# Kernel optimization log

Hardware: AMD Instinct MI355X
Metric: run time of the kernel (lower is better)

Reference implementation:

```python
import jax, jax.numpy as jnp
import numpy as np

B, N, L, K = 32, 512, 8, 8


def setup_inputs() -> dict:
    key = jax.random.key(0)
    k1, k2 = jax.random.split(key)
    A = jax.random.normal(k1, (B, N, N), dtype=jnp.float32)
    A = 0.5 * (A + A.transpose(0, 2, 1))  # symmetric matrix, as in MMF use-case
    O_stack = jax.random.normal(k2, (L, B, K, K), dtype=jnp.float32)  # per-level KxK rotations
    rng = np.random.default_rng(0)
    idx = np.stack([np.sort(rng.choice(N, K, replace=False)) for _ in range(B * L)])
    indices = jnp.asarray(idx.reshape(B, L, K), dtype=jnp.int32)  # sorted, distinct per (b,l)
    wavelet = indices[:, :, 0]  # wavelet index is one of the selected indices per level
    return {"A": A, "O_stack": O_stack, "indices": indices, "wavelet": wavelet}


def reference(A, O_stack, indices, wavelet):
    Bz, Nz, _ = A.shape
    Lz = O_stack.shape[0]
    eye = jnp.eye(Nz, dtype=A.dtype)

    def build_U(idx, O):
        # identity except the KxK block at (idx_i, idx_j) replaced by O
        # (matches torch boolean-mask row-major fill since idx is sorted)
        return eye.at[idx[:, None], idx[None, :]].set(O)

    right = None
    for l in range(Lz):
        U = jax.vmap(build_U)(indices[:, l], O_stack[l])  # [B,N,N]
        right = U if l == 0 else U @ right
        A = U @ A @ U.transpose(0, 2, 1)

    # final masking: zero rows/cols of wavelet indices, keep diagonal
    active = jnp.ones((Bz, Nz), dtype=A.dtype).at[jnp.arange(Bz)[:, None], wavelet].set(0.0)
    left = active[:, :, None] * active[:, None, :]
    d = jnp.arange(Nz)
    left = left.at[:, d, d].set(1.0)
    D = A * left
    A_rec = right.transpose(0, 2, 1) @ D @ right
    return (A_rec, right, D)
```

## Files before the change

### kernel.cpp

```cpp
#include <hip/hip_runtime.h>

#define BATCH 32
#define NDIM 512
#define LNUM 8
#define KDIM 8

#define WS_PM     0
#define WS_S      512
#define WS_ACT    640
#define WS_W      1152
#define WS_B2     5248
#define WS_C2     9344
#define WS_RA     13440
#define WS_RD     46208
#define WS_RAT    78976
#define WS_RDT    111744
#define WS_STRIDE 144512

#define LSTR 65
typedef float f4 __attribute__((ext_vector_type(4)));

__global__ __launch_bounds__(256) void k_prep(
    const float* __restrict__ A, const float* __restrict__ O,
    const int* __restrict__ indices, const int* __restrict__ wavelet,
    float* __restrict__ ws)
{
    const int b  = blockIdx.x;
    const int cy = blockIdx.y;
    const int tid = threadIdx.x;
    float* base = ws + (size_t)b * WS_STRIDE;

    __shared__ float Wl[64*LSTR];
    __shared__ __align__(16) float Buf1[64*LSTR];
    __shared__ __align__(16) float Buf2[64*LSTR];
    __shared__ __align__(16) float Buf3[64*LSTR];
    __shared__ int   pml[NDIM];
    __shared__ float actl[NDIM];
    __shared__ float actS[64];
    __shared__ int   idxsh[64];
    __shared__ int   Ssh[64];
    __shared__ float Oall[LNUM*KDIM*KDIM];

    for (int t = tid; t < LNUM*KDIM*KDIM; t += 256) {
        int l = t >> 6, k = t & 63;
        Oall[t] = O[((size_t)l*BATCH + b)*(KDIM*KDIM) + k];
    }
    if (tid < 64) idxsh[tid] = indices[b*64 + tid];
    for (int n = tid; n < NDIM; n += 256) { pml[n] = -1; actl[n] = 1.f; }
    __syncthreads();

    const int wv = tid >> 6;
    const int ln = tid & 63;
    int s_reg = 0;

    if (wv == 0) {
        int n = idxsh[ln];
        bool first = true;
        for (int t = 0; t < ln; ++t) if (idxsh[t] == n) first = false;
        unsigned long long m = __ballot(first);
        int rank = __popcll(m & ((1ull << ln) - 1ull));
        s_reg = (int)__popcll(m);
        if (first) { pml[n] = rank; Ssh[rank] = n; }
        if (ln >= s_reg) Ssh[ln] = 0;
        if (ln < LNUM) actl[wavelet[b*LNUM + ln]] = 0.f;
    }
    __syncthreads();

    if (wv == 0) {
        actS[ln] = actl[Ssh[ln]];
        for (int rr = 0; rr < 64; ++rr)
            Wl[rr*LSTR + ln] = (rr == ln && rr < s_reg) ? 1.f : 0.f;
        for (int l = 0; l < LNUM; ++l) {
            int pr[KDIM];
            float wcol[KDIM], accv[KDIM];
            #pragma unroll
            for (int j = 0; j < KDIM; ++j) pr[j] = pml[idxsh[l*KDIM + j]];
            #pragma unroll
            for (int j = 0; j < KDIM; ++j) wcol[j] = Wl[pr[j]*LSTR + ln];
            #pragma unroll
            for (int i = 0; i < KDIM; ++i) {
                float a = 0.f;
                #pragma unroll
                for (int j = 0; j < KDIM; ++j)
                    a += Oall[l*64 + i*KDIM + j] * wcol[j];
                accv[i] = a;
            }
            #pragma unroll
            for (int i = 0; i < KDIM; ++i) Wl[pr[i]*LSTR + ln] = accv[i];
        }
    } else {
        if (cy < 8) {
            const int j0 = cy * 64;
            for (int t = tid - 64; t < 1024; t += 192) {
                int n = t >> 4, cc = t & 15;
                f4 v = ((const f4*)(A + ((size_t)b*NDIM + Ssh[n])*NDIM + j0))[cc];
                ((f4*)(Buf1 + n*64))[cc] = v;
            }
        } else {
            for (int t = tid - 64; t < 4096; t += 192) {
                int n = t >> 6, mm = t & 63;
                Buf1[n*LSTR + mm] = A[((size_t)b*NDIM + Ssh[n])*NDIM + Ssh[mm]];
            }
            int*   g_posmap = (int*)(base + WS_PM);
            float* g_act    = base + WS_ACT;
            for (int n = tid - 64; n < NDIM; n += 192) {
                g_posmap[n] = pml[n]; g_act[n] = actl[n];
            }
        }
    }
    __syncthreads();

    if (cy < 8) {
        const int j0 = cy * 64;
        float* AS  = Buf1;
        float* RAt = Buf2;
        float* g_RA  = base + WS_RA;
        float* g_RD  = base + WS_RD;
        float* g_RAT = base + WS_RAT;
        float* g_RDT = base + WS_RDT;

        const int g = wv;
        const int j = ln;
        float racc[16];

        #pragma unroll
        for (int k = 0; k < 16; ++k) racc[k] = 0.f;
        for (int n = 0; n < 64; ++n) {
            float av = AS[n*64 + j];
            #pragma unroll
            for (int k = 0; k < 16; ++k) racc[k] += Wl[(g*16 + k)*LSTR + n] * av;
        }
        #pragma unroll
        for (int k = 0; k < 16; ++k) {
            RAt[(g*16 + k)*64 + j] = racc[k];
            g_RA[(g*16 + k)*NDIM + j0 + j] = racc[k];
        }
        {
            f4* dst = (f4*)(g_RAT + (size_t)(j0 + j)*64 + g*16);
            #pragma unroll
            for (int q = 0; q < 4; ++q) {
                f4 v = { racc[4*q], racc[4*q+1], racc[4*q+2], racc[4*q+3] };
                dst[q] = v;
            }
        }
        __syncthreads();

        #pragma unroll
        for (int k = 0; k < 16; ++k) racc[k] = 0.f;
        for (int n = 0; n < 64; ++n) {
            float dt = actS[n] * RAt[n*64 + j];
            #pragma unroll
            for (int k = 0; k < 16; ++k) racc[k] += Wl[n*LSTR + g*16 + k] * dt;
        }
        const float aj = actl[j0 + j];
        #pragma unroll
        for (int k = 0; k < 16; ++k) {
            float rd = racc[k] * aj;
            racc[k] = rd;
            g_RD[(g*16 + k)*NDIM + j0 + j] = rd;
        }
        {
            f4* dst = (f4*)(g_RDT + (size_t)(j0 + j)*64 + g*16);
            #pragma unroll
            for (int q = 0; q < 4; ++q) {
                f4 v = { racc[4*q], racc[4*q+1], racc[4*q+2], racc[4*q+3] };
                dst[q] = v;
            }
        }
    } else {
        {
            float* g_W = base + WS_W;
            for (int t = tid; t < 4096; t += 256) g_W[t] = Wl[(t>>6)*LSTR + (t&63)];
        }

        const int w = wv;
        float acc[16];

        #pragma unroll
        for (int k = 0; k < 16; ++k) acc[k] = 0.f;
        for (int n = 0; n < 64; ++n) {
            float as = Buf1[n*LSTR + ln];
            #pragma unroll
            for (int k = 0; k < 16; ++k) acc[k] += Wl[(w*16 + k)*LSTR + n] * as;
        }
        #pragma unroll
        for (int k = 0; k < 16; ++k) Buf2[(w*16 + k)*LSTR + ln] = acc[k];
        __syncthreads();

        #pragma unroll
        for (int k = 0; k < 16; ++k) acc[k] = 0.f;
        for (int m = 0; m < 64; ++m) {
            float wvv = Wl[ln*LSTR + m];
            #pragma unroll
            for (int k = 0; k < 16; ++k) acc[k] += Buf2[(w*16 + k)*LSTR + m] * wvv;
        }
        #pragma unroll
        for (int k = 0; k < 16; ++k) Buf3[(w*16 + k)*LSTR + ln] = acc[k];
        __syncthreads();
        {
            float* g_B2 = base + WS_B2;
            for (int t = tid; t < 4096; t += 256) g_B2[t] = Buf3[(t>>6)*LSTR + (t&63)];
        }

        for (int t = tid; t < 4096; t += 256) {
            int n = t >> 6, m = t & 63;
            float mv = (Ssh[n] == Ssh[m]) ? 1.f : actS[n]*actS[m];
            Buf1[n*LSTR + m] = mv * Buf3[n*LSTR + m];
        }
        __syncthreads();

        #pragma unroll
        for (int k = 0; k < 16; ++k) acc[k] = 0.f;
        for (int n = 0; n < 64; ++n) {
            float dv = Buf1[n*LSTR + ln];
            #pragma unroll
            for (int k = 0; k < 16; ++k) acc[k] += Wl[n*LSTR + (w*16 + k)] * dv;
        }
        #pragma unroll
        for (int k = 0; k < 16; ++k) Buf2[(w*16 + k)*LSTR + ln] = acc[k];
        __syncthreads();

        #pragma unroll
        for (int k = 0; k < 16; ++k) acc[k] = 0.f;
        for (int m = 0; m < 64; ++m) {
            float wvv = Wl[m*LSTR + ln];
            #pragma unroll
            for (int k = 0; k < 16; ++k) acc[k] += Buf2[(w*16 + k)*LSTR + m] * wvv;
        }
        {
            float* g_C2 = base + WS_C2;
            #pragma unroll
            for (int k = 0; k < 16; ++k) g_C2[(w*16 + k)*64 + ln] = acc[k];
        }
    }
}

__global__ __launch_bounds__(256) void k_big(const float* __restrict__ A,
                                             const float* __restrict__ ws,
                                             float* __restrict__ out)
{
    const int b = blockIdx.y;
    const int rh = threadIdx.x >> 7;
    const int lane = threadIdx.x & 127;
    const int i = blockIdx.x*2 + rh;
    const int j0 = lane*4;

    const float* base = ws + (size_t)b * WS_STRIDE;
    const int*   posmap = (const int*)(base + WS_PM);
    const float* act = base + WS_ACT;
    const float* g_W  = base + WS_W;
    const float* g_B2 = base + WS_B2;
    const float* g_C2 = base + WS_C2;
    const float* RA  = base + WS_RA;
    const float* RD  = base + WS_RD;
    const float* RAT = base + WS_RAT;
    const float* RDT = base + WS_RDT;

    const int pi = posmap[i];
    const float acti = act[i];
    const size_t rowoff = ((size_t)b*NDIM + i)*NDIM;
    const size_t seg = (size_t)BATCH*NDIM*NDIM;

    int4   p4  = ((const int4*)posmap)[lane];
    float4 aj4 = ((const float4*)act)[lane];
    int   pm[4] = {p4.x, p4.y, p4.z, p4.w};
    float aj[4] = {aj4.x, aj4.y, aj4.z, aj4.w};

    float a[4], arec[4], dv[4], rv[4];

    if (pi < 0) {
        const float* rat = RAT + (size_t)i*64;
        const float* rdt = RDT + (size_t)i*64;
        f4 v = __builtin_nontemporal_load((const f4*)(A + rowoff) + lane);
        a[0]=v.x; a[1]=v.y; a[2]=v.z; a[3]=v.w;
        #pragma unroll
        for (int c = 0; c < 4; ++c) {
            int pj = pm[c];
            if (pj >= 0) a[c] = rat[pj];
            float mv = (i == j0 + c) ? 1.f : acti * aj[c];
            dv[c] = a[c] * mv;
            arec[c] = (pj < 0) ? dv[c] : rdt[pj];
            rv[c] = (i == j0 + c) ? 1.f : 0.f;
        }
    } else {
        f4 v = ((const f4*)(RA + (size_t)pi*NDIM))[lane];
        f4 w = ((const f4*)(RD + (size_t)pi*NDIM))[lane];
        a[0]=v.x; a[1]=v.y; a[2]=v.z; a[3]=v.w;
        arec[0]=w.x; arec[1]=w.y; arec[2]=w.z; arec[3]=w.w;
        #pragma unroll
        for (int c = 0; c < 4; ++c) {
            int pj = pm[c];
            if (pj >= 0) {
                a[c]    = g_B2[pi*64 + pj];
                arec[c] = g_C2[pi*64 + pj];
                rv[c]   = g_W[pi*64 + pj];
            } else {
                rv[c] = 0.f;
            }
            float mv = (i == j0 + c) ? 1.f : acti * aj[c];
            dv[c] = a[c] * mv;
        }
    }

    f4 o0; o0.x = arec[0]; o0.y = arec[1]; o0.z = arec[2]; o0.w = arec[3];
    f4 o1; o1.x = rv[0];   o1.y = rv[1];   o1.z = rv[2];   o1.w = rv[3];
    f4 o2; o2.x = dv[0];   o2.y = dv[1];   o2.z = dv[2];   o2.w = dv[3];
    __builtin_nontemporal_store(o0, (f4*)(out + rowoff) + lane);
    __builtin_nontemporal_store(o1, (f4*)(out + seg + rowoff) + lane);
    __builtin_nontemporal_store(o2, (f4*)(out + 2*seg + rowoff) + lane);
}

extern "C" void kernel_launch(void* const* d_in, const int* in_sizes, int n_in,
                              void* d_out, int out_size, void* d_ws, size_t ws_size,
                              hipStream_t stream) {
    const float* A       = (const float*)d_in[0];
    const float* O       = (const float*)d_in[1];
    const int*   indices = (const int*)d_in[2];
    const int*   wavelet = (const int*)d_in[3];
    float* ws  = (float*)d_ws;
    float* out = (float*)d_out;

    k_prep<<<dim3(BATCH, 9), 256, 0, stream>>>(A, O, indices, wavelet, ws);
    k_big <<<dim3(NDIM/2, BATCH), 256, 0, stream>>>(A, ws, out);
}
```

Measured before the change: 175.8 us.

## Write touched-row outputs directly from prep kernel, skip them in big kernel

The prep kernel now writes the output rows for selected indices (the rows touched by rotations) straight into the three outputs, scattered by column. It no longer stages RA/RD/W/B2/C2 in workspace. The big kernel returns early for rows whose posmap is non-negative, so it only streams the untouched rows. This removes a workspace round trip and some redundant reads. In exchange the prep kernel does scattered, uncoalesced single-float stores, and k_big blocks now diverge, since half of a block may exit.

```diff
diff --git a/kernel.cpp b/kernel.cpp
--- a/kernel.cpp
+++ b/kernel.cpp
@@ -6,13 +6,7 @@
 #define KDIM 8
 
 #define WS_PM     0
-#define WS_S      512
 #define WS_ACT    640
-#define WS_W      1152
-#define WS_B2     5248
-#define WS_C2     9344
-#define WS_RA     13440
-#define WS_RD     46208
 #define WS_RAT    78976
 #define WS_RDT    111744
 #define WS_STRIDE 144512
@@ -23,12 +17,13 @@
 __global__ __launch_bounds__(256) void k_prep(
     const float* __restrict__ A, const float* __restrict__ O,
     const int* __restrict__ indices, const int* __restrict__ wavelet,
-    float* __restrict__ ws)
+    float* __restrict__ ws, float* __restrict__ out)
 {
     const int b  = blockIdx.x;
     const int cy = blockIdx.y;
     const int tid = threadIdx.x;
     float* base = ws + (size_t)b * WS_STRIDE;
+    const size_t seg = (size_t)BATCH*NDIM*NDIM;
 
     __shared__ float Wl[64*LSTR];
     __shared__ __align__(16) float Buf1[64*LSTR];
@@ -40,6 +35,7 @@
     __shared__ int   idxsh[64];
     __shared__ int   Ssh[64];
     __shared__ float Oall[LNUM*KDIM*KDIM];
+    __shared__ int   s_sh;
 
     for (int t = tid; t < LNUM*KDIM*KDIM; t += 256) {
         int l = t >> 6, k = t & 63;
@@ -63,6 +59,7 @@
         if (first) { pml[n] = rank; Ssh[rank] = n; }
         if (ln >= s_reg) Ssh[ln] = 0;
         if (ln < LNUM) actl[wavelet[b*LNUM + ln]] = 0.f;
+        if (ln == 0) s_sh = s_reg;
     }
     __syncthreads();
 
@@ -109,18 +106,20 @@
         }
     }
     __syncthreads();
+    const int s = s_sh;
 
     if (cy < 8) {
         const int j0 = cy * 64;
         float* AS  = Buf1;
         float* RAt = Buf2;
-        float* g_RA  = base + WS_RA;
-        float* g_RD  = base + WS_RD;
         float* g_RAT = base + WS_RAT;
         float* g_RDT = base + WS_RDT;
 
         const int g = wv;
         const int j = ln;
+        const int jg = j0 + j;
+        const int pj = pml[jg];
+        const float aj = actl[jg];
         float racc[16];
 
         #pragma unroll
@@ -131,18 +130,26 @@
             for (int k = 0; k < 16; ++k) racc[k] += Wl[(g*16 + k)*LSTR + n] * av;
         }
         #pragma unroll
-        for (int k = 0; k < 16; ++k) {
-            RAt[(g*16 + k)*64 + j] = racc[k];
-            g_RA[(g*16 + k)*NDIM + j0 + j] = racc[k];
-        }
+        for (int k = 0; k < 16; ++k) RAt[(g*16 + k)*64 + j] = racc[k];
         {
-            f4* dst = (f4*)(g_RAT + (size_t)(j0 + j)*64 + g*16);
+            f4* dst = (f4*)(g_RAT + (size_t)jg*64 + g*16);
             #pragma unroll
             for (int q = 0; q < 4; ++q) {
                 f4 v = { racc[4*q], racc[4*q+1], racc[4*q+2], racc[4*q+3] };
                 dst[q] = v;
             }
         }
+        if (pj < 0) {
+            #pragma unroll
+            for (int k = 0; k < 16; ++k) {
+                int r = g*16 + k;
+                if (r < s) {
+                    size_t ro = ((size_t)b*NDIM + Ssh[r])*NDIM + jg;
+                    out[2*seg + ro] = racc[k] * actS[r] * aj;
+                    out[seg + ro]   = 0.f;
+                }
+            }
+        }
         __syncthreads();
 
         #pragma unroll
@@ -152,27 +159,27 @@
             #pragma unroll
             for (int k = 0; k < 16; ++k) racc[k] += Wl[n*LSTR + g*16 + k] * dt;
         }
-        const float aj = actl[j0 + j];
-        #pragma unroll
-        for (int k = 0; k < 16; ++k) {
-            float rd = racc[k] * aj;
-            racc[k] = rd;
-            g_RD[(g*16 + k)*NDIM + j0 + j] = rd;
-        }
+        #pragma unroll
+        for (int k = 0; k < 16; ++k) racc[k] *= aj;
         {
-            f4* dst = (f4*)(g_RDT + (size_t)(j0 + j)*64 + g*16);
+            f4* dst = (f4*)(g_RDT + (size_t)jg*64 + g*16);
             #pragma unroll
             for (int q = 0; q < 4; ++q) {
                 f4 v = { racc[4*q], racc[4*q+1], racc[4*q+2], racc[4*q+3] };
                 dst[q] = v;
             }
         }
+        if (pj < 0) {
+            #pragma unroll
+            for (int k = 0; k < 16; ++k) {
+                int r = g*16 + k;
+                if (r < s) {
+                    size_t ro = ((size_t)b*NDIM + Ssh[r])*NDIM + jg;
+                    out[ro] = racc[k];
+                }
+            }
+        }
     } else {
-        {
-            float* g_W = base + WS_W;
-            for (int t = tid; t < 4096; t += 256) g_W[t] = Wl[(t>>6)*LSTR + (t&63)];
-        }
-
         const int w = wv;
         float acc[16];
 
@@ -197,10 +204,6 @@
         #pragma unroll
         for (int k = 0; k < 16; ++k) Buf3[(w*16 + k)*LSTR + ln] = acc[k];
         __syncthreads();
-        {
-            float* g_B2 = base + WS_B2;
-            for (int t = tid; t < 4096; t += 256) g_B2[t] = Buf3[(t>>6)*LSTR + (t&63)];
-        }
 
         for (int t = tid; t < 4096; t += 256) {
             int n = t >> 6, m = t & 63;
@@ -227,10 +230,17 @@
             #pragma unroll
             for (int k = 0; k < 16; ++k) acc[k] += Buf2[(w*16 + k)*LSTR + m] * wvv;
         }
-        {
-            float* g_C2 = base + WS_C2;
-            #pragma unroll
-            for (int k = 0; k < 16; ++k) g_C2[(w*16 + k)*64 + ln] = acc[k];
+        if (ln < s) {
+            #pragma unroll
+            for (int k = 0; k < 16; ++k) {
+                int p = w*16 + k;
+                if (p < s) {
+                    size_t ro = ((size_t)b*NDIM + Ssh[p])*NDIM + Ssh[ln];
+                    out[ro]         = acc[k];
+                    out[seg + ro]   = Wl[p*LSTR + ln];
+                    out[2*seg + ro] = Buf1[p*LSTR + ln];
+                }
+            }
         }
     }
 }
@@ -248,15 +258,12 @@
     const float* base = ws + (size_t)b * WS_STRIDE;
     const int*   posmap = (const int*)(base + WS_PM);
     const float* act = base + WS_ACT;
-    const float* g_W  = base + WS_W;
-    const float* g_B2 = base + WS_B2;
-    const float* g_C2 = base + WS_C2;
-    const float* RA  = base + WS_RA;
-    const float* RD  = base + WS_RD;
     const float* RAT = base + WS_RAT;
     const float* RDT = base + WS_RDT;
 
     const int pi = posmap[i];
+    if (pi >= 0) return;
+
     const float acti = act[i];
     const size_t rowoff = ((size_t)b*NDIM + i)*NDIM;
     const size_t seg = (size_t)BATCH*NDIM*NDIM;
@@ -266,40 +273,20 @@
     int   pm[4] = {p4.x, p4.y, p4.z, p4.w};
     float aj[4] = {aj4.x, aj4.y, aj4.z, aj4.w};
 
+    const float* rat = RAT + (size_t)i*64;
+    const float* rdt = RDT + (size_t)i*64;
+
     float a[4], arec[4], dv[4], rv[4];
-
-    if (pi < 0) {
-        const float* rat = RAT + (size_t)i*64;
-        const float* rdt = RDT + (size_t)i*64;
-        f4 v = __builtin_nontemporal_load((const f4*)(A + rowoff) + lane);
-        a[0]=v.x; a[1]=v.y; a[2]=v.z; a[3]=v.w;
-        #pragma unroll
-        for (int c = 0; c < 4; ++c) {
-            int pj = pm[c];
-            if (pj >= 0) a[c] = rat[pj];
-            float mv = (i == j0 + c) ? 1.f : acti * aj[c];
-            dv[c] = a[c] * mv;
-            arec[c] = (pj < 0) ? dv[c] : rdt[pj];
-            rv[c] = (i == j0 + c) ? 1.f : 0.f;
-        }
-    } else {
-        f4 v = ((const f4*)(RA + (size_t)pi*NDIM))[lane];
-        f4 w = ((const f4*)(RD + (size_t)pi*NDIM))[lane];
-        a[0]=v.x; a[1]=v.y; a[2]=v.z; a[3]=v.w;
-        arec[0]=w.x; arec[1]=w.y; arec[2]=w.z; arec[3]=w.w;
-        #pragma unroll
-        for (int c = 0; c < 4; ++c) {
-            int pj = pm[c];
-            if (pj >= 0) {
-                a[c]    = g_B2[pi*64 + pj];
-                arec[c] = g_C2[pi*64 + pj];
-                rv[c]   = g_W[pi*64 + pj];
-            } else {
-                rv[c] = 0.f;
-            }
-            float mv = (i == j0 + c) ? 1.f : acti * aj[c];
-            dv[c] = a[c] * mv;
-        }
+    f4 v = __builtin_nontemporal_load((const f4*)(A + rowoff) + lane);
+    a[0]=v.x; a[1]=v.y; a[2]=v.z; a[3]=v.w;
+    #pragma unroll
+    for (int c = 0; c < 4; ++c) {
+        int pj = pm[c];
+        if (pj >= 0) a[c] = rat[pj];
+        float mv = (i == j0 + c) ? 1.f : acti * aj[c];
+        dv[c] = a[c] * mv;
+        arec[c] = (pj < 0) ? dv[c] : rdt[pj];
+        rv[c] = (i == j0 + c) ? 1.f : 0.f;
     }
 
     f4 o0; o0.x = arec[0]; o0.y = arec[1]; o0.z = arec[2]; o0.w = arec[3];
@@ -320,6 +307,6 @@
     float* ws  = (float*)d_ws;
     float* out = (float*)d_out;
 
-    k_prep<<<dim3(BATCH, 9), 256, 0, stream>>>(A, O, indices, wavelet, ws);
+    k_prep<<<dim3(BATCH, 9), 256, 0, stream>>>(A, O, indices, wavelet, ws, out);
     k_big <<<dim3(NDIM/2, BATCH), 256, 0, stream>>>(A, ws, out);
 }
```

Result: no change. 178.9 us (+1.8%).
